# Kernel optimization log

Hardware: AMD Instinct MI355X
Metric: run time of the kernel (lower is better)

Reference implementation:

```python
import jax, jax.numpy as jnp
import numpy as np
from jax import lax

B, C, H, W = 32, 3, 128, 128   # batch, image channels, event spatial dims
PC = 16                         # conditioning distribution_params channels
HID = 64                        # hidden channels of each parallel CNN
NUP = 2                         # number of upsampling stages
DN = ('NCHW', 'OIHW', 'NCHW')

BASE_SLICE = (slice(0, None, 2), slice(0, None, 2))
UP_SLICES = [(slice(1, None, 2), slice(1, None, 2)),
             (slice(0, None, 2), slice(1, None, 2)),
             (slice(1, None, 2), slice(0, None, 2))]


def setup_inputs() -> dict:
    key = jax.random.key(0)
    k0, k1, k2, k3 = jax.random.split(key, 4)
    n_nets = C + NUP * 3 * C  # 3 base + 18 upsampling nets = 21
    cin = C + PC
    return {
        'value': jax.random.uniform(k0, (B, C, H, W), jnp.float32),
        'distribution_params': jax.random.normal(k1, (B, PC, H, W), jnp.float32),
        'W1': jax.random.normal(k2, (n_nets, HID, cin, 3, 3), jnp.float32) * 0.05,
        'b1': jnp.zeros((n_nets, HID), jnp.float32),
        'W2': jax.random.normal(k3, (n_nets, 1, HID, 1, 1), jnp.float32) * 0.05,
        'b2': jnp.zeros((n_nets, 1), jnp.float32),
    }


def _cnn(x, w1, bb1, w2, bb2):
    # Conv3x3 -> ReLU -> Conv1x1, producing Bernoulli logits [B,1,h,w]
    h = lax.conv_general_dilated(x, w1, (1, 1), 'SAME', dimension_numbers=DN)
    h = jax.nn.relu(h + bb1[None, :, None, None])
    o = lax.conv_general_dilated(h, w2, (1, 1), 'SAME', dimension_numbers=DN)
    return o + bb2[None, :, None, None]


def _log_prob_block(imgs, params, masked, sl, idxs, W1, b1, W2, b2):
    lp = jnp.float32(0.0)
    for c, idx in enumerate(idxs):
        net_in = jnp.concatenate([masked, params], axis=1)
        logits = _cnn(net_in, W1[idx], b1[idx], W2[idx], b2[idx])[:, 0, sl[0], sl[1]]
        x = imgs[:, c, sl[0], sl[1]]
        # Bernoulli log-prob with logits, summed over batch and spatial dims
        lp = lp + jnp.sum(x * jax.nn.log_sigmoid(logits)
                          + (1.0 - x) * jax.nn.log_sigmoid(-logits))
        masked = masked.at[:, c, sl[0], sl[1]].set(x)
    return lp, masked


def reference(value, distribution_params, W1, b1, W2, b2):
    r = 2 ** NUP
    base = value[:, :, ::r, ::r]
    base_dp = distribution_params[:, :, ::r, ::r]
    masked = jnp.zeros_like(base)
    lp, masked = _log_prob_block(base, base_dp, masked, BASE_SLICE,
                                 list(range(C)), W1, b1, W2, b2)
    for level in range(NUP):
        rr = 2 ** (NUP - level - 1)
        v = value[:, :, ::rr, ::rr]
        dp = distribution_params[:, :, ::rr, ::rr]
        m = jnp.zeros_like(v)
        m = m.at[:, :, BASE_SLICE[0], BASE_SLICE[1]].set(
            v[:, :, BASE_SLICE[0], BASE_SLICE[1]])
        for s in range(3):
            idxs = [C + level * 3 * C + s * C + c for c in range(C)]
            blp, m = _log_prob_block(v, dp, m, UP_SLICES[s], idxs, W1, b1, W2, b2)
            lp = lp + blp
    return lp
```

## Files before the change

kernel.cpp:

```cpp
#include <hip/hip_runtime.h>

typedef unsigned char uchar;
typedef unsigned long long ull;
typedef __attribute__((ext_vector_type(2))) unsigned long long ullx2;
typedef __attribute__((ext_vector_type(4))) float floatx4;
typedef __attribute__((ext_vector_type(4))) unsigned int uintx4;

#define NB_IMG 18496
#define WHALF 9216
#define AREG 16352

__device__ __forceinline__ uchar f2e4(float x) {
    float a = fabsf(x);
    unsigned s = (__float_as_uint(x) >> 24) & 0x80u;
    if (a >= 448.f) return (uchar)(s | 0x7E);
    if (a < 0.015625f) {
        int m = (int)rintf(a * 512.f);
        return (uchar)(s | (unsigned)m);
    }
    unsigned u = __float_as_uint(a);
    unsigned r = u + 0x7FFFFu + ((u >> 20) & 1u);
    unsigned e8 = (r >> 23) - 120u;
    return (uchar)(s | (e8 << 3) | ((r >> 20) & 7u));
}

__device__ __forceinline__ float row16sum(float v) {
    v += __int_as_float(__builtin_amdgcn_update_dpp(0, __float_as_int(v), 0x128, 0xf, 0xf, false));
    v += __int_as_float(__builtin_amdgcn_update_dpp(0, __float_as_int(v), 0x124, 0xf, 0xf, false));
    v += __int_as_float(__builtin_amdgcn_update_dpp(0, __float_as_int(v), 0x122, 0xf, 0xf, false));
    v += __int_as_float(__builtin_amdgcn_update_dpp(0, __float_as_int(v), 0x121, 0xf, 0xf, false));
    return v;
}

__device__ __forceinline__ void eval_geom(int e, int& sy0, int& sx0, int& cch, int& s_idx) {
    if (e < 3) { sy0 = 0; sx0 = 0; cch = e; s_idx = -1; }
    else {
        int u = e - 3; int s = (u % 9) / 3; cch = u % 3; s_idx = s;
        sy0 = (s == 1) ? 0 : 1;
        sx0 = (s == 2) ? 0 : 1;
    }
}

__device__ __forceinline__ bool tap_active(int e, int ci, int dy, int dx,
                                           int sy0, int sx0, int cch, int s_idx) {
    if (ci >= 3) return true;
    int py = (sy0 + dy - 1) & 1;
    int px = (sx0 + dx - 1) & 1;
    if (e < 3) return (py == 0 && px == 0) && (ci < cch);
    if (py == 0 && px == 0) return true;
    int sp = (py == 1 && px == 1) ? 0 : ((py == 0 && px == 1) ? 1 : 2);
    return (sp < s_idx) || (sp == s_idx && ci < cch);
}

__global__ __launch_bounds__(256) void prep_kernel(
    const float* __restrict__ value, const float* __restrict__ dp,
    const float* __restrict__ W1,
    uchar* __restrict__ imgbf, uchar* __restrict__ wbfA, uchar* __restrict__ wbfB)
{
    const int bid = blockIdx.x;
    if (bid < 2312) {
        const int t = bid * 256 + threadIdx.x;
        const int b = t / NB_IMG;
        const int r = t - b * NB_IMG;
        const int y = r / 136;
        const int rr = r - y * 136;
        const int p = rr / 68;
        const int xh = rr - p * 68;
        const int yi = y - 4;
        const int xi = 2 * (xh - 2) + p;
        unsigned d[8];
        #pragma unroll
        for (int i = 0; i < 8; ++i) d[i] = 0;
        if ((unsigned)yi < 128u && (unsigned)xi < 128u) {
            const int o = yi * 128 + xi;
            const float* vb = value + (size_t)b * 3 * 16384 + o;
            const float* pb = dp + (size_t)b * 16 * 16384 + o;
            #pragma unroll
            for (int i = 0; i < 3; ++i) d[i >> 2] |= (unsigned)f2e4(vb[i * 16384]) << ((i & 3) * 8);
            #pragma unroll
            for (int i = 0; i < 16; ++i) {
                const int ci = 3 + i;
                d[ci >> 2] |= (unsigned)f2e4(pb[i * 16384]) << ((ci & 3) * 8);
            }
        }
        uchar* dst = imgbf + (size_t)t * 32;
        uintx4 v0, v1;
        v0[0] = d[0]; v0[1] = d[1]; v0[2] = d[2]; v0[3] = d[3];
        v1[0] = d[4]; v1[1] = d[5]; v1[2] = d[6]; v1[3] = d[7];
        *(uintx4*)dst = v0;
        *(uintx4*)(dst + 16) = v1;
    } else {
        const int q = bid - 2312;
        const int e = q / 9, tap = q % 9;
        const int g = threadIdx.x >> 6, n = threadIdx.x & 63;
        int sy0, sx0, cch, s_idx;
        eval_geom(e, sy0, sx0, cch, s_idx);
        const int dy = tap / 3, dx = tap % 3;
        const float* wrow = W1 + ((size_t)e * 64 + n) * 171;
        ull v = 0;
        #pragma unroll
        for (int qq = 0; qq < 8; ++qq) {
            const int ci = g * 8 + qq;
            float w = 0.f;
            if (ci < 19 && tap_active(e, ci, dy, dx, sy0, sx0, cch, s_idx))
                w = wrow[ci * 9 + tap];
            v |= (ull)f2e4(w) << (qq * 8);
        }
        if (n < 32) *(ull*)&wbfA[(size_t)e * WHALF + ((tap * 4 + g) * 32 + n) * 8] = v;
        else        *(ull*)&wbfB[(size_t)e * WHALF + ((tap * 4 + g) * 32 + (n - 32)) * 8] = v;
    }
}

struct SW { ullx2 a, b, c; };

__device__ __forceinline__ void sw_load(int tid, SW& r, const uchar* wbfB, int e) {
    const uchar* src = wbfB + (size_t)e * WHALF;
    r.a = *(const ullx2*)(src + tid * 16);
    r.b = *(const ullx2*)(src + (256 + tid) * 16);
    if (tid < 64) r.c = *(const ullx2*)(src + (512 + tid) * 16);
}
__device__ __forceinline__ void sw_write(int tid, uchar* dst, const SW& r) {
    *(ullx2*)(dst + tid * 16) = r.a;
    *(ullx2*)(dst + (256 + tid) * 16) = r.b;
    if (tid < 64) *(ullx2*)(dst + (512 + tid) * 16) = r.c;
}

template<int SY0, int SX0, int RSH, int OWSH, int TXH>
__device__ __forceinline__ void class_body(
    int e0, int e_after, int& buf, float& lpsum,
    int b, int oy0, int ox0, int tid,
    const uchar* Alds, uchar* Wb0, uchar* Wb1,
    const uchar* __restrict__ wbfA, const uchar* __restrict__ wbfB,
    const float* __restrict__ value, const float* __restrict__ b1,
    const float* __restrict__ W2, const float* __restrict__ b2)
{
    constexpr int OW = 1 << OWSH;
    const int w = tid >> 6, lane = tid & 63, l15 = lane & 15, l4 = lane >> 4;
    int abase[2];
    #pragma unroll
    for (int a = 0; a < 2; ++a) {
        const int row = w * 32 + a * 16 + l15;
        const int oy = row >> OWSH, ox = row & (OW - 1);
        abase[a] = ((SY0 + 2 * oy) * 2 * TXH + ox) * 24 + l4 * 8;
    }
    const int wfb = l4 * 256 + l15 * 8;

    #pragma unroll 1
    for (int c = 0; c < 3; ++c) {
        const int e = e0 + c;
        __syncthreads();
        uchar* Wcur = buf ? Wb1 : Wb0;
        uchar* Wnxt = buf ? Wb0 : Wb1;
        const int en = (c < 2) ? (e + 1) : e_after;

        SW sw;
        if (en >= 0) sw_load(tid, sw, wbfB, en);

        const uchar* wA = wbfA + (size_t)e * WHALF;
        ull breg[9][2];
        #pragma unroll
        for (int tap = 0; tap < 9; ++tap) {
            breg[tap][0] = *(const ull*)(wA + tap * 1024 + wfb);
            breg[tap][1] = *(const ull*)(wA + tap * 1024 + wfb + 128);
        }
        float b1c[4], w2c[4];
        #pragma unroll
        for (int nb = 0; nb < 4; ++nb) {
            b1c[nb] = b1[e * 64 + nb * 16 + l15];
            w2c[nb] = W2[e * 64 + nb * 16 + l15];
        }
        const float bias2 = b2[e];

        floatx4 acc[2][4];
        #pragma unroll
        for (int a = 0; a < 2; ++a)
            #pragma unroll
            for (int nb = 0; nb < 4; ++nb)
                acc[a][nb] = (floatx4){0.f, 0.f, 0.f, 0.f};

        __builtin_amdgcn_s_setprio(1);
        #pragma unroll
        for (int tap = 0; tap < 9; ++tap) {
            const int dy = tap / 3, dx = tap % 3;
            const int v = SX0 + dx + 1;
            const int D = (2 * dy + (v & 1)) * TXH + (v >> 1);
            ull av[2];
            #pragma unroll
            for (int a = 0; a < 2; ++a)
                av[a] = *(const ull*)(Alds + abase[a] + D * 24);
            const ull bv2 = *(const ull*)(Wcur + wfb + tap * 1024);
            const ull bv3 = *(const ull*)(Wcur + wfb + tap * 1024 + 128);
            #pragma unroll
            for (int a = 0; a < 2; ++a) {
                acc[a][0] = __builtin_amdgcn_mfma_f32_16x16x32_fp8_fp8((long)av[a], (long)breg[tap][0], acc[a][0], 0, 0, 0);
                acc[a][1] = __builtin_amdgcn_mfma_f32_16x16x32_fp8_fp8((long)av[a], (long)breg[tap][1], acc[a][1], 0, 0, 0);
                acc[a][2] = __builtin_amdgcn_mfma_f32_16x16x32_fp8_fp8((long)av[a], (long)bv2, acc[a][2], 0, 0, 0);
                acc[a][3] = __builtin_amdgcn_mfma_f32_16x16x32_fp8_fp8((long)av[a], (long)bv3, acc[a][3], 0, 0, 0);
            }
        }
        __builtin_amdgcn_s_setprio(0);

        float zv[8];
        #pragma unroll
        for (int a = 0; a < 2; ++a)
            #pragma unroll
            for (int j = 0; j < 4; ++j) {
                float part = 0.f;
                #pragma unroll
                for (int nb = 0; nb < 4; ++nb)
                    part += w2c[nb] * fmaxf(acc[a][nb][j] + b1c[nb], 0.f);
                zv[a * 4 + j] = row16sum(part);
            }
        if (l15 < 8) {
            const float u0 = (l15 & 1) ? zv[1] : zv[0];
            const float u1 = (l15 & 1) ? zv[3] : zv[2];
            const float u2 = (l15 & 1) ? zv[5] : zv[4];
            const float u3 = (l15 & 1) ? zv[7] : zv[6];
            const float p0 = (l15 & 2) ? u1 : u0;
            const float p1 = (l15 & 2) ? u3 : u2;
            const float zs = ((l15 & 4) ? p1 : p0) + bias2;
            const int row = w * 32 + ((l15 >> 2) << 4) + (l4 << 2) + (l15 & 3);
            const int oyj = oy0 + (row >> OWSH);
            const int oxj = ox0 + (row & (OW - 1));
            const int yj = (SY0 + 2 * oyj) << RSH;
            const int xj = (SX0 + 2 * oxj) << RSH;
            const float xv = value[((size_t)b * 3 + c) * 16384 + yj * 128 + xj];
            const float az = fabsf(zs);
            const float t2 = __builtin_amdgcn_exp2f(-1.442695041f * az);
            const float l1p = 0.69314718056f * __builtin_amdgcn_logf(1.f + t2);
            lpsum += xv * zs + fminf(-zs, 0.f) - l1p;
        }

        if (en >= 0) sw_write(tid, Wnxt, sw);
        buf ^= 1;
    }
}

template<int EB, int RSH, int OWSH, int TXH, int TY, int NCLS>
__device__ __forceinline__ void run_level(
    int b, int oy0, int ox0, int tid,
    uchar* Alds, uchar* Wb0, uchar* Wb1, float* wsum,
    const uchar* __restrict__ imgbf, const uchar* __restrict__ wbfA,
    const uchar* __restrict__ wbfB, const float* __restrict__ value,
    const float* __restrict__ b1, const float* __restrict__ W2,
    const float* __restrict__ b2, float* __restrict__ out)
{
    constexpr int TPIX = TY * 2 * TXH;
    const int lane = tid & 63, w = tid >> 6;

    SW sw0;
    sw_load(tid, sw0, wbfB, EB);

    const int yb = 2 * oy0 - 1, xb = 2 * ox0 - 2;
    const uchar* img_b = imgbf + (size_t)b * ((size_t)NB_IMG * 32);
    #pragma unroll
    for (int i = 0; i < (TPIX + 255) / 256; ++i) {
        const int px = tid + i * 256;
        if (px < TPIX) {
            const int typ = px / TXH;
            const int xh = px - typ * TXH;
            const int yl = yb + (typ >> 1);
            const int xl = xb + 2 * xh + (typ & 1);
            int yi = (yl << RSH) + 4; yi = yi < 0 ? 0 : (yi > 135 ? 135 : yi);
            int xi = (xl << RSH) + 4; xi = xi < 0 ? 0 : (xi > 135 ? 135 : xi);
            const uchar* src = img_b + (size_t)(yi * 136 + (xi & 1) * 68 + (xi >> 1)) * 32;
            ullx2 v01 = *(const ullx2*)src;
            ull v2 = *(const ull*)(src + 16);
            uchar* dst = Alds + px * 24;
            *(ull*)dst = v01[0];
            *(ull*)(dst + 8) = v01[1];
            *(ull*)(dst + 16) = v2;
        }
    }
    if (tid < 4) *(ull*)(Alds + TPIX * 24 + tid * 8) = 0ull;
    sw_write(tid, Wb0, sw0);

    int buf = 0;
    float lpsum = 0.f;
    if constexpr (NCLS == 3) {
        class_body<1, 1, RSH, OWSH, TXH>(EB + 0, EB + 3, buf, lpsum, b, oy0, ox0, tid, Alds, Wb0, Wb1, wbfA, wbfB, value, b1, W2, b2);
        class_body<0, 1, RSH, OWSH, TXH>(EB + 3, EB + 6, buf, lpsum, b, oy0, ox0, tid, Alds, Wb0, Wb1, wbfA, wbfB, value, b1, W2, b2);
        class_body<1, 0, RSH, OWSH, TXH>(EB + 6, -1, buf, lpsum, b, oy0, ox0, tid, Alds, Wb0, Wb1, wbfA, wbfB, value, b1, W2, b2);
    } else {
        class_body<0, 0, RSH, OWSH, TXH>(EB, -1, buf, lpsum, b, oy0, ox0, tid, Alds, Wb0, Wb1, wbfA, wbfB, value, b1, W2, b2);
    }

    lpsum += __shfl_down(lpsum, 32);
    lpsum += __shfl_down(lpsum, 16);
    lpsum += __shfl_down(lpsum, 8);
    lpsum += __shfl_down(lpsum, 4);
    lpsum += __shfl_down(lpsum, 2);
    lpsum += __shfl_down(lpsum, 1);
    if (lane == 0) wsum[w] = lpsum;
    __syncthreads();
    if (tid == 0) atomicAdd(out, wsum[0] + wsum[1] + wsum[2] + wsum[3]);
}

__global__ __launch_bounds__(256, 4) void pcnn_all(
    const uchar* __restrict__ imgbf, const uchar* __restrict__ wbfA,
    const uchar* __restrict__ wbfB, const float* __restrict__ value,
    const float* __restrict__ b1, const float* __restrict__ W2,
    const float* __restrict__ b2, float* __restrict__ out)
{
    __shared__ __align__(16) uchar Alds[AREG];
    __shared__ __align__(16) uchar Wb0[WHALF];
    __shared__ __align__(16) uchar Wb1[WHALF];
    __shared__ float wsum[4];
    const int bid = blockIdx.x, tid = threadIdx.x;

    const int x = bid & 7, r = bid >> 3;
    const int g = r / 42, u = r - g * 42;
    const int b = g * 8 + x;

    if (u < 32) {
        run_level<12, 0, 5, 34, 10, 3>(b, (u >> 1) * 4, (u & 1) * 32, tid, Alds, Wb0, Wb1, wsum,
                                       imgbf, wbfA, wbfB, value, b1, W2, b2, out);
    } else if (u < 40) {
        run_level<3, 1, 5, 34, 10, 3>(b, (u - 32) * 4, 0, tid, Alds, Wb0, Wb1, wsum,
                                      imgbf, wbfA, wbfB, value, b1, W2, b2, out);
    } else {
        run_level<0, 2, 4, 17, 18, 1>(b, (u - 40) * 8, 0, tid, Alds, Wb0, Wb1, wsum,
                                      imgbf, wbfA, wbfB, value, b1, W2, b2, out);
    }
}

extern "C" void kernel_launch(void* const* d_in, const int* in_sizes, int n_in,
                              void* d_out, int out_size, void* d_ws, size_t ws_size,
                              hipStream_t stream) {
    const float* value = (const float*)d_in[0];
    const float* dp    = (const float*)d_in[1];
    const float* W1    = (const float*)d_in[2];
    const float* b1    = (const float*)d_in[3];
    const float* W2    = (const float*)d_in[4];
    const float* b2    = (const float*)d_in[5];
    float* out = (float*)d_out;

    uchar* imgbf = (uchar*)d_ws;
    uchar* wbfA  = imgbf + (size_t)32 * NB_IMG * 32;
    uchar* wbfB  = wbfA + (size_t)21 * WHALF;

    hipMemsetAsync(out, 0, sizeof(float), stream);
    hipLaunchKernelGGL(prep_kernel, dim3(2501), dim3(256), 0, stream,
                       value, dp, W1, imgbf, wbfA, wbfB);
    hipLaunchKernelGGL(pcnn_all, dim3(1344), dim3(256), 0, stream,
                       imgbf, wbfA, wbfB, value, b1, W2, b2, out);
}
```

Baseline: 81.41 us.

## Single-buffer LDS weight half to raise occupancy; zero output in prep kernel

Replaces the double-buffered LDS weight staging with one buffer. Each iteration now writes the prefetched register copy into LDS between two barriers, then issues the next prefetch. Shared memory per block drops from roughly 35KB to 26KB, and launch bounds go from 4 to 6 blocks per SM to raise occupancy. The hipMemsetAsync that cleared the output is removed, and the prep kernel zeroes it instead, saving one launch. The cost is an extra barrier per channel and less overlap between the weight store and compute.

```diff
diff --git a/kernel.cpp b/kernel.cpp
--- a/kernel.cpp
+++ b/kernel.cpp
@@ -55,7 +55,8 @@
 __global__ __launch_bounds__(256) void prep_kernel(
     const float* __restrict__ value, const float* __restrict__ dp,
     const float* __restrict__ W1,
-    uchar* __restrict__ imgbf, uchar* __restrict__ wbfA, uchar* __restrict__ wbfB)
+    uchar* __restrict__ imgbf, uchar* __restrict__ wbfA, uchar* __restrict__ wbfB,
+    float* __restrict__ out)
 {
     const int bid = blockIdx.x;
     if (bid < 2312) {
@@ -108,6 +109,7 @@
         }
         if (n < 32) *(ull*)&wbfA[(size_t)e * WHALF + ((tap * 4 + g) * 32 + n) * 8] = v;
         else        *(ull*)&wbfB[(size_t)e * WHALF + ((tap * 4 + g) * 32 + (n - 32)) * 8] = v;
+        if (bid == 2500 && threadIdx.x == 0) out[0] = 0.f;
     }
 }
 
@@ -127,9 +129,9 @@
 
 template<int SY0, int SX0, int RSH, int OWSH, int TXH>
 __device__ __forceinline__ void class_body(
-    int e0, int e_after, int& buf, float& lpsum,
+    int e0, int e_after, SW& sw, float& lpsum,
     int b, int oy0, int ox0, int tid,
-    const uchar* Alds, uchar* Wb0, uchar* Wb1,
+    const uchar* Alds, uchar* Wb,
     const uchar* __restrict__ wbfA, const uchar* __restrict__ wbfB,
     const float* __restrict__ value, const float* __restrict__ b1,
     const float* __restrict__ W2, const float* __restrict__ b2)
@@ -148,13 +150,12 @@
     #pragma unroll 1
     for (int c = 0; c < 3; ++c) {
         const int e = e0 + c;
+        const int en = (c < 2) ? (e + 1) : e_after;
+
         __syncthreads();
-        uchar* Wcur = buf ? Wb1 : Wb0;
-        uchar* Wnxt = buf ? Wb0 : Wb1;
-        const int en = (c < 2) ? (e + 1) : e_after;
-
-        SW sw;
+        sw_write(tid, Wb, sw);
         if (en >= 0) sw_load(tid, sw, wbfB, en);
+        __syncthreads();
 
         const uchar* wA = wbfA + (size_t)e * WHALF;
         ull breg[9][2];
@@ -188,8 +189,8 @@
             #pragma unroll
             for (int a = 0; a < 2; ++a)
                 av[a] = *(const ull*)(Alds + abase[a] + D * 24);
-            const ull bv2 = *(const ull*)(Wcur + wfb + tap * 1024);
-            const ull bv3 = *(const ull*)(Wcur + wfb + tap * 1024 + 128);
+            const ull bv2 = *(const ull*)(Wb + wfb + tap * 1024);
+            const ull bv3 = *(const ull*)(Wb + wfb + tap * 1024 + 128);
             #pragma unroll
             for (int a = 0; a < 2; ++a) {
                 acc[a][0] = __builtin_amdgcn_mfma_f32_16x16x32_fp8_fp8((long)av[a], (long)breg[tap][0], acc[a][0], 0, 0, 0);
@@ -230,16 +231,13 @@
             const float l1p = 0.69314718056f * __builtin_amdgcn_logf(1.f + t2);
             lpsum += xv * zs + fminf(-zs, 0.f) - l1p;
         }
-
-        if (en >= 0) sw_write(tid, Wnxt, sw);
-        buf ^= 1;
     }
 }
 
 template<int EB, int RSH, int OWSH, int TXH, int TY, int NCLS>
 __device__ __forceinline__ void run_level(
     int b, int oy0, int ox0, int tid,
-    uchar* Alds, uchar* Wb0, uchar* Wb1, float* wsum,
+    uchar* Alds, uchar* Wb, float* wsum,
     const uchar* __restrict__ imgbf, const uchar* __restrict__ wbfA,
     const uchar* __restrict__ wbfB, const float* __restrict__ value,
     const float* __restrict__ b1, const float* __restrict__ W2,
@@ -248,8 +246,8 @@
     constexpr int TPIX = TY * 2 * TXH;
     const int lane = tid & 63, w = tid >> 6;
 
-    SW sw0;
-    sw_load(tid, sw0, wbfB, EB);
+    SW sw;
+    sw_load(tid, sw, wbfB, EB);
 
     const int yb = 2 * oy0 - 1, xb = 2 * ox0 - 2;
     const uchar* img_b = imgbf + (size_t)b * ((size_t)NB_IMG * 32);
@@ -273,16 +271,14 @@
         }
     }
     if (tid < 4) *(ull*)(Alds + TPIX * 24 + tid * 8) = 0ull;
-    sw_write(tid, Wb0, sw0);
-
-    int buf = 0;
+
     float lpsum = 0.f;
     if constexpr (NCLS == 3) {
-        class_body<1, 1, RSH, OWSH, TXH>(EB + 0, EB + 3, buf, lpsum, b, oy0, ox0, tid, Alds, Wb0, Wb1, wbfA, wbfB, value, b1, W2, b2);
-        class_body<0, 1, RSH, OWSH, TXH>(EB + 3, EB + 6, buf, lpsum, b, oy0, ox0, tid, Alds, Wb0, Wb1, wbfA, wbfB, value, b1, W2, b2);
-        class_body<1, 0, RSH, OWSH, TXH>(EB + 6, -1, buf, lpsum, b, oy0, ox0, tid, Alds, Wb0, Wb1, wbfA, wbfB, value, b1, W2, b2);
+        class_body<1, 1, RSH, OWSH, TXH>(EB + 0, EB + 3, sw, lpsum, b, oy0, ox0, tid, Alds, Wb, wbfA, wbfB, value, b1, W2, b2);
+        class_body<0, 1, RSH, OWSH, TXH>(EB + 3, EB + 6, sw, lpsum, b, oy0, ox0, tid, Alds, Wb, wbfA, wbfB, value, b1, W2, b2);
+        class_body<1, 0, RSH, OWSH, TXH>(EB + 6, -1, sw, lpsum, b, oy0, ox0, tid, Alds, Wb, wbfA, wbfB, value, b1, W2, b2);
     } else {
-        class_body<0, 0, RSH, OWSH, TXH>(EB, -1, buf, lpsum, b, oy0, ox0, tid, Alds, Wb0, Wb1, wbfA, wbfB, value, b1, W2, b2);
+        class_body<0, 0, RSH, OWSH, TXH>(EB, -1, sw, lpsum, b, oy0, ox0, tid, Alds, Wb, wbfA, wbfB, value, b1, W2, b2);
     }
 
     lpsum += __shfl_down(lpsum, 32);
@@ -296,15 +292,14 @@
     if (tid == 0) atomicAdd(out, wsum[0] + wsum[1] + wsum[2] + wsum[3]);
 }
 
-__global__ __launch_bounds__(256, 4) void pcnn_all(
+__global__ __launch_bounds__(256, 6) void pcnn_all(
     const uchar* __restrict__ imgbf, const uchar* __restrict__ wbfA,
     const uchar* __restrict__ wbfB, const float* __restrict__ value,
     const float* __restrict__ b1, const float* __restrict__ W2,
     const float* __restrict__ b2, float* __restrict__ out)
 {
     __shared__ __align__(16) uchar Alds[AREG];
-    __shared__ __align__(16) uchar Wb0[WHALF];
-    __shared__ __align__(16) uchar Wb1[WHALF];
+    __shared__ __align__(16) uchar Wb[WHALF];
     __shared__ float wsum[4];
     const int bid = blockIdx.x, tid = threadIdx.x;
 
@@ -313,13 +308,13 @@
     const int b = g * 8 + x;
 
     if (u < 32) {
-        run_level<12, 0, 5, 34, 10, 3>(b, (u >> 1) * 4, (u & 1) * 32, tid, Alds, Wb0, Wb1, wsum,
+        run_level<12, 0, 5, 34, 10, 3>(b, (u >> 1) * 4, (u & 1) * 32, tid, Alds, Wb, wsum,
                                        imgbf, wbfA, wbfB, value, b1, W2, b2, out);
     } else if (u < 40) {
-        run_level<3, 1, 5, 34, 10, 3>(b, (u - 32) * 4, 0, tid, Alds, Wb0, Wb1, wsum,
+        run_level<3, 1, 5, 34, 10, 3>(b, (u - 32) * 4, 0, tid, Alds, Wb, wsum,
                                       imgbf, wbfA, wbfB, value, b1, W2, b2, out);
     } else {
-        run_level<0, 2, 4, 17, 18, 1>(b, (u - 40) * 8, 0, tid, Alds, Wb0, Wb1, wsum,
+        run_level<0, 2, 4, 17, 18, 1>(b, (u - 40) * 8, 0, tid, Alds, Wb, wsum,
                                       imgbf, wbfA, wbfB, value, b1, W2, b2, out);
     }
 }
@@ -339,9 +334,8 @@
     uchar* wbfA  = imgbf + (size_t)32 * NB_IMG * 32;
     uchar* wbfB  = wbfA + (size_t)21 * WHALF;
 
-    hipMemsetAsync(out, 0, sizeof(float), stream);
     hipLaunchKernelGGL(prep_kernel, dim3(2501), dim3(256), 0, stream,
-                       value, dp, W1, imgbf, wbfA, wbfB);
+                       value, dp, W1, imgbf, wbfA, wbfB, out);
     hipLaunchKernelGGL(pcnn_all, dim3(1344), dim3(256), 0, stream,
                        imgbf, wbfA, wbfB, value, b1, W2, b2, out);
 }
```

After: 170.0 us. 109% more time.
